# Kernel tuning notes

Measured on AMD Instinct MI355X. Metric: run time of the kernel, lower is better.

The kernel has to match this reference:

```python
import jax, jax.numpy as jnp
import numpy as np

N_USERS = 100000
N_ITEMS = 50000
N_NODES = N_USERS + N_ITEMS
NNZ = 1600000          # user-item interactions
EMBED_DIM = 64
N_LAYERS = 3
NORM_EPS = 1e-12       # F.normalize eps
DEG_EPS = 1e-07        # degree eps from module


def _build_graph():
    rng = np.random.default_rng(0)
    u = rng.integers(0, N_USERS, NNZ)
    v = rng.integers(0, N_ITEMS, NNZ)
    # dedupe (row, col) pairs so COO has unique entries, matching (A>0) degree logic
    pair = np.unique(u.astype(np.int64) * N_ITEMS + v.astype(np.int64))
    u = (pair // N_ITEMS).astype(np.int32)
    v = (pair % N_ITEMS).astype(np.int32)
    rows = np.concatenate([u, v + N_USERS]).astype(np.int32)
    cols = np.concatenate([v + N_USERS, u]).astype(np.int32)
    deg = np.bincount(rows, minlength=N_NODES).astype(np.float32)
    dinv = np.power(deg + DEG_EPS, -0.5).astype(np.float32)
    vals = dinv[rows] * dinv[cols]
    return rows, cols, vals


def setup_inputs() -> dict:
    key = jax.random.key(0)
    rows, cols, vals = _build_graph()
    in_embs = jax.random.normal(key, (N_NODES, EMBED_DIM), dtype=jnp.float32)
    return {
        "in_embs": in_embs,
        "rows": jnp.asarray(rows),
        "cols": jnp.asarray(cols),
        "vals": jnp.asarray(vals),
    }


def reference(in_embs, rows, cols, vals):
    n = in_embs.shape[0]
    x = in_embs
    out = in_embs
    for i in range(N_LAYERS):
        # SpMM: A_norm @ x  via edge gather + segment_sum scatter
        msg = vals[:, None] * x[cols]                      # [E, d]
        x = jax.ops.segment_sum(msg, rows, num_segments=n)  # [n, d]
        # F.normalize(x, dim=-1)
        norm = jnp.linalg.norm(x, axis=-1, keepdims=True)
        x = x / jnp.maximum(norm, NORM_EPS)
        out = out + x / (i + 1)
    return out
```

## Files before the change

### kernel.cpp

```cpp
#include <hip/hip_runtime.h>
#include <hip/hip_bf16.h>


constexpr int N_USERS = 100000;
constexpr int N_ITEMS = 50000;
constexpr int N_NODES = N_USERS + N_ITEMS;
constexpr int D = 64;
constexpr int NBK  = 196;
constexpr int SLOT = 12288;
constexpr int EPB  = 16384;

__device__ inline unsigned short f2bf(float f) {
    unsigned u = __float_as_uint(f);
    u += 0x7FFFu + ((u >> 16) & 1u);
    return (unsigned short)(u >> 16);
}
__device__ inline float bf2f(unsigned short h) {
    return __uint_as_float((unsigned)h << 16);
}

__global__ __launch_bounds__(256) void rpu_kernel(
    const int* __restrict__ rows, int* __restrict__ rpu, int Eh)
{
    int i = blockIdx.x * 256 + threadIdx.x;
    if (i > N_USERS) return;
    int lo = 0, hi = Eh;
    while (lo < hi) {
        int mid = (lo + hi) >> 1;
        if (rows[mid] < i) lo = mid + 1; else hi = mid;
    }
    rpu[i] = lo;
}

__global__ __launch_bounds__(256) void dinv_users(
    const int* __restrict__ rpu, float* __restrict__ dinv)
{
    int i = blockIdx.x * 256 + threadIdx.x;
    if (i < N_USERS)
        dinv[i] = rsqrtf((float)(rpu[i + 1] - rpu[i]) + 1e-7f);
}

__global__ __launch_bounds__(256) void init_cursors(int* __restrict__ bcur)
{
    int t = threadIdx.x;
    if (t < NBK) bcur[t] = t * SLOT;
}

__global__ __launch_bounds__(256) void bucket_scatter(
    const int* __restrict__ rows, const int* __restrict__ cols,
    int* __restrict__ bcur, int* __restrict__ staging, int Eh)
{
    __shared__ int hist[256];
    const int tid = threadIdx.x;
    const int base = blockIdx.x * EPB;
    const int nEdge = min(EPB, Eh - base);
    if (nEdge <= 0) return;

    hist[tid] = 0;
    __syncthreads();

    for (int s = 0; s < 16; ++s) {
        int o = s * 1024 + tid * 4;
        if (o + 3 < nEdge) {
            int4 c4 = *reinterpret_cast<const int4*>(cols + base + o);
            atomicAdd(&hist[(c4.x - N_USERS) >> 8], 1);
            atomicAdd(&hist[(c4.y - N_USERS) >> 8], 1);
            atomicAdd(&hist[(c4.z - N_USERS) >> 8], 1);
            atomicAdd(&hist[(c4.w - N_USERS) >> 8], 1);
        } else if (o < nEdge) {
            for (int k = o; k < nEdge; ++k)
                atomicAdd(&hist[(cols[base + k] - N_USERS) >> 8], 1);
        }
    }
    __syncthreads();

    if (tid < NBK) {
        int h = hist[tid];
        hist[tid] = (h > 0) ? atomicAdd(&bcur[tid], h) : 0;
    }
    __syncthreads();

    for (int s = 0; s < 16; ++s) {
        int o = s * 1024 + tid * 4;
        if (o + 3 < nEdge) {
            int4 c4 = *reinterpret_cast<const int4*>(cols + base + o);
            int4 u4 = *reinterpret_cast<const int4*>(rows + base + o);
            int v, p;
            v = c4.x - N_USERS; p = atomicAdd(&hist[v >> 8], 1);
            staging[p] = ((v & 255) << 24) | u4.x;
            v = c4.y - N_USERS; p = atomicAdd(&hist[v >> 8], 1);
            staging[p] = ((v & 255) << 24) | u4.y;
            v = c4.z - N_USERS; p = atomicAdd(&hist[v >> 8], 1);
            staging[p] = ((v & 255) << 24) | u4.z;
            v = c4.w - N_USERS; p = atomicAdd(&hist[v >> 8], 1);
            staging[p] = ((v & 255) << 24) | u4.w;
        } else if (o < nEdge) {
            for (int k = o; k < nEdge; ++k) {
                int v = cols[base + k] - N_USERS;
                int u = rows[base + k];
                int p = atomicAdd(&hist[v >> 8], 1);
                staging[p] = ((v & 255) << 24) | u;
            }
        }
    }
}

__global__ __launch_bounds__(256) void scan_buckets(
    const int* __restrict__ bcur, int* __restrict__ bbase, int* __restrict__ rpi)
{
    __shared__ int wsum[4];
    const int tid = threadIdx.x, lane = tid & 63, w = tid >> 6;
    int t = (tid < NBK) ? (bcur[tid] - tid * SLOT) : 0;
    int incl = t;
    #pragma unroll
    for (int off = 1; off < 64; off <<= 1) {
        int s = __shfl_up(incl, off);
        if (lane >= off) incl += s;
    }
    if (lane == 63) wsum[w] = incl;
    __syncthreads();
    int woff = 0;
    #pragma unroll
    for (int k = 0; k < 4; ++k) woff += (k < w) ? wsum[k] : 0;
    int excl = woff + incl - t;
    if (tid < NBK) bbase[tid] = excl;
    if (tid == NBK - 1) rpi[N_ITEMS] = excl + t;
}

__global__ __launch_bounds__(256) void item_csr(
    const int* __restrict__ bcur, const int* __restrict__ bbase,
    const int* __restrict__ staging, int* __restrict__ rpi,
    float* __restrict__ dinv, int* __restrict__ csr)
{
    __shared__ int hist[256];
    __shared__ int cur[256];
    __shared__ int wsum[4];
    const int b = blockIdx.x;
    const int tid = threadIdx.x, lane = tid & 63, w = tid >> 6;
    const int sbase = b * SLOT;
    const int n = bcur[b] - sbase;
    const int cbase = bbase[b];

    hist[tid] = 0;
    __syncthreads();
    for (int i = tid; i < n; i += 256)
        atomicAdd(&hist[((unsigned)staging[sbase + i]) >> 24], 1);
    __syncthreads();

    int h = hist[tid];
    int incl = h;
    #pragma unroll
    for (int off = 1; off < 64; off <<= 1) {
        int s = __shfl_up(incl, off);
        if (lane >= off) incl += s;
    }
    if (lane == 63) wsum[w] = incl;
    __syncthreads();
    int woff = 0;
    #pragma unroll
    for (int k = 0; k < 4; ++k) woff += (k < w) ? wsum[k] : 0;
    int excl = woff + incl - h;

    int gitem = b * 256 + tid;
    if (gitem < N_ITEMS) {
        rpi[gitem] = cbase + excl;
        dinv[N_USERS + gitem] = rsqrtf((float)h + 1e-7f);
    }
    cur[tid] = cbase + excl;
    __syncthreads();

    for (int i = tid; i < n; i += 256) {
        int e = staging[sbase + i];
        int p = atomicAdd(&cur[((unsigned)e) >> 24], 1);
        csr[p] = e & 0xFFFFFF;
    }
}

__global__ __launch_bounds__(256) void prep0(
    const float* __restrict__ init, const float* __restrict__ dinv,
    unsigned short* __restrict__ z)
{
    int i = blockIdx.x * 256 + threadIdx.x;
    if (i >= N_NODES * D / 4) return;
    int r = i >> 4;
    float dv = dinv[r];
    float4 x = reinterpret_cast<const float4*>(init)[i];
    ushort4 o;
    o.x = f2bf(x.x * dv); o.y = f2bf(x.y * dv);
    o.z = f2bf(x.z * dv); o.w = f2bf(x.w * dv);
    reinterpret_cast<ushort4*>(z)[i] = o;
}

__global__ __launch_bounds__(256) void spmm_norm(
    const unsigned short* __restrict__ z,
    const int* __restrict__ rpu,
    const int* __restrict__ rpi,
    const int* __restrict__ cols_u,
    const int* __restrict__ csr_col_i,
    const float* __restrict__ dinv,
    const float* __restrict__ init,
    unsigned short* __restrict__ zout,
    float* __restrict__ out,
    float invl, int first, int writez)
{
    const int tid = threadIdx.x;
    const int lane = tid & 63;
    const int g = lane >> 4;
    const int sl = lane & 15;
    const int wave = tid >> 6;
    const int row = blockIdx.x * 16 + wave * 4 + g;
    if (row >= N_NODES) return;
    const int gb = g << 4;

    int beg, end;
    const int* clist;
    if (row < N_USERS) {
        beg = rpu[row]; end = rpu[row + 1]; clist = cols_u;
    } else {
        int v = row - N_USERS;
        beg = rpi[v]; end = rpi[v + 1]; clist = csr_col_i;
    }

    float ax = 0.f, ay = 0.f, az = 0.f, aw = 0.f;
    for (int base = beg; base < end; base += 16) {
        int li = base + sl;
        int c_l = 0;
        if (li < end) c_l = clist[li];
        int nch = min(16, end - base);
        int j = 0;
        for (; j + 4 <= nch; j += 4) {
            int c0 = __shfl(c_l, gb + j + 0);
            int c1 = __shfl(c_l, gb + j + 1);
            int c2 = __shfl(c_l, gb + j + 2);
            int c3 = __shfl(c_l, gb + j + 3);
            ushort4 z0 = reinterpret_cast<const ushort4*>(z + (size_t)c0 * D)[sl];
            ushort4 z1 = reinterpret_cast<const ushort4*>(z + (size_t)c1 * D)[sl];
            ushort4 z2 = reinterpret_cast<const ushort4*>(z + (size_t)c2 * D)[sl];
            ushort4 z3 = reinterpret_cast<const ushort4*>(z + (size_t)c3 * D)[sl];
            ax += bf2f(z0.x); ay += bf2f(z0.y); az += bf2f(z0.z); aw += bf2f(z0.w);
            ax += bf2f(z1.x); ay += bf2f(z1.y); az += bf2f(z1.z); aw += bf2f(z1.w);
            ax += bf2f(z2.x); ay += bf2f(z2.y); az += bf2f(z2.z); aw += bf2f(z2.w);
            ax += bf2f(z3.x); ay += bf2f(z3.y); az += bf2f(z3.z); aw += bf2f(z3.w);
        }
        for (; j < nch; ++j) {
            int c = __shfl(c_l, gb + j);
            ushort4 zv = reinterpret_cast<const ushort4*>(z + (size_t)c * D)[sl];
            ax += bf2f(zv.x); ay += bf2f(zv.y); az += bf2f(zv.z); aw += bf2f(zv.w);
        }
    }

    float ss = ax * ax + ay * ay + az * az + aw * aw;
    #pragma unroll
    for (int off = 8; off > 0; off >>= 1)
        ss += __shfl_xor(ss, off);
    float nrm = sqrtf(ss);
    float rinv = 1.0f / fmaxf(nrm, 1e-12f);

    float xnx = ax * rinv, xny = ay * rinv, xnz = az * rinv, xnw = aw * rinv;

    size_t idx = (size_t)row * D + sl * 4;
    if (writez) {
        float dv = dinv[row];
        ushort4 zo;
        zo.x = f2bf(xnx * dv); zo.y = f2bf(xny * dv);
        zo.z = f2bf(xnz * dv); zo.w = f2bf(xnw * dv);
        reinterpret_cast<ushort4*>(zout + (size_t)row * D)[sl] = zo;
    }

    float4 bo = first ? *reinterpret_cast<const float4*>(init + idx)
                      : *reinterpret_cast<const float4*>(out + idx);
    bo.x += xnx * invl; bo.y += xny * invl;
    bo.z += xnz * invl; bo.w += xnw * invl;
    *reinterpret_cast<float4*>(out + idx) = bo;
}

extern "C" void kernel_launch(void* const* d_in, const int* in_sizes, int n_in,
                              void* d_out, int out_size, void* d_ws, size_t ws_size,
                              hipStream_t stream) {
    const float* in_embs = (const float*)d_in[0];
    const int*   rows    = (const int*)d_in[1];
    const int*   cols    = (const int*)d_in[2];
    float* out = (float*)d_out;

    const int E  = in_sizes[1];
    const int Eh = E / 2;
    const size_t z_bytes = (size_t)N_NODES * D * sizeof(unsigned short);

    auto align256 = [](size_t x) { return (x + 255) & ~(size_t)255; };
    char* p = (char*)d_ws;
    unsigned short* zP = (unsigned short*)p; p += align256(z_bytes);
    unsigned short* zQ = (unsigned short*)p; p += align256(z_bytes);
    int*   csr_col_i = (int*)p;   p += align256((size_t)Eh * sizeof(int));
    int*   rpu       = (int*)p;   p += align256((size_t)(N_USERS + 1) * sizeof(int));
    int*   rpi       = (int*)p;   p += align256((size_t)(N_ITEMS + 1) * sizeof(int));
    float* dinv      = (float*)p; p += align256((size_t)N_NODES * sizeof(float));
    int*   bcur      = (int*)p;   p += align256(256 * sizeof(int));
    int*   bbase     = (int*)p;   p += align256(256 * sizeof(int));
    int*   staging   = (int*)zP;

    init_cursors<<<1, 256, 0, stream>>>(bcur);
    bucket_scatter<<<(Eh + EPB - 1) / EPB, 256, 0, stream>>>(rows, cols, bcur, staging, Eh);
    scan_buckets<<<1, 256, 0, stream>>>(bcur, bbase, rpi);
    item_csr<<<NBK, 256, 0, stream>>>(bcur, bbase, staging, rpi, dinv, csr_col_i);
    rpu_kernel<<<(N_USERS + 256) / 256, 256, 0, stream>>>(rows, rpu, Eh);
    dinv_users<<<(N_USERS + 255) / 256, 256, 0, stream>>>(rpu, dinv);
    prep0<<<(N_NODES * D / 4 + 255) / 256, 256, 0, stream>>>(in_embs, dinv, zP);

    const int spmm_blocks = (N_NODES + 15) / 16;
    unsigned short* zin = zP;
    unsigned short* zout = zQ;
    for (int layer = 0; layer < 3; ++layer) {
        int last = (layer == 2);
        spmm_norm<<<spmm_blocks, 256, 0, stream>>>(
            zin, rpu, rpi, cols, csr_col_i, dinv, in_embs, zout, out,
            1.0f / (layer + 1), layer == 0 ? 1 : 0, last ? 0 : 1);
        unsigned short* t = zin; zin = zout; zout = t;
    }
}
```

Before: 250.7 us.

## Defer output accumulation to last layer, widen SpMM gathers, and fuse setup kernels

The SpMM kernel now assigns 8 lanes per row, each loading 16 bytes of bf16 features, so each gathered row takes fewer, wider memory instructions. The running fp32 output is no longer read and written after every layer. The final layer instead rebuilds the layer-1 and layer-2 embeddings from the stored bf16 z buffers by dividing out dinv, and writes the whole sum once. Several small setup kernels are merged: cursor init and user dinv move into rpu_kernel, and the bucket scan moves into item_csr. The cost is extra error, because the earlier layers' contributions now come from bf16 values scaled by 1/dinv rather than fp32.

```diff
diff --git a/kernel.cpp b/kernel.cpp
--- a/kernel.cpp
+++ b/kernel.cpp
@@ -10,40 +10,35 @@
 constexpr int SLOT = 12288;
 constexpr int EPB  = 16384;
 
-__device__ inline unsigned short f2bf(float f) {
+__device__ inline unsigned f2bf(float f) {
     unsigned u = __float_as_uint(f);
     u += 0x7FFFu + ((u >> 16) & 1u);
-    return (unsigned short)(u >> 16);
-}
-__device__ inline float bf2f(unsigned short h) {
-    return __uint_as_float((unsigned)h << 16);
+    return u >> 16;
+}
+__device__ inline float bflo(unsigned u) { return __uint_as_float(u << 16); }
+__device__ inline float bfhi(unsigned u) { return __uint_as_float(u & 0xFFFF0000u); }
+
+__device__ inline int lower_bound(const int* __restrict__ a, int n, int key) {
+    int lo = 0, hi = n;
+    while (lo < hi) { int m = (lo + hi) >> 1; if (a[m] < key) lo = m + 1; else hi = m; }
+    return lo;
 }
 
 __global__ __launch_bounds__(256) void rpu_kernel(
-    const int* __restrict__ rows, int* __restrict__ rpu, int Eh)
-{
+    const int* __restrict__ rows, int* __restrict__ rpu,
+    float* __restrict__ dinv, int* __restrict__ bcur, int Eh)
+{
+    if (blockIdx.x == 0 && threadIdx.x < NBK) bcur[threadIdx.x] = threadIdx.x * SLOT;
     int i = blockIdx.x * 256 + threadIdx.x;
     if (i > N_USERS) return;
-    int lo = 0, hi = Eh;
-    while (lo < hi) {
-        int mid = (lo + hi) >> 1;
-        if (rows[mid] < i) lo = mid + 1; else hi = mid;
-    }
+    int lo = lower_bound(rows, Eh, i);
     rpu[i] = lo;
-}
-
-__global__ __launch_bounds__(256) void dinv_users(
-    const int* __restrict__ rpu, float* __restrict__ dinv)
-{
-    int i = blockIdx.x * 256 + threadIdx.x;
+    int lane = threadIdx.x & 63;
+    int nxt = __shfl_down(lo, 1);
+    if (lane == 63 || i >= N_USERS)
+        nxt = (i < N_USERS) ? lower_bound(rows, Eh, i + 1) : lo;
     if (i < N_USERS)
-        dinv[i] = rsqrtf((float)(rpu[i + 1] - rpu[i]) + 1e-7f);
-}
-
-__global__ __launch_bounds__(256) void init_cursors(int* __restrict__ bcur)
-{
-    int t = threadIdx.x;
-    if (t < NBK) bcur[t] = t * SLOT;
+        dinv[i] = rsqrtf((float)(nxt - lo) + 1e-7f);
 }
 
 __global__ __launch_bounds__(256) void bucket_scatter(
@@ -105,13 +100,19 @@
     }
 }
 
-__global__ __launch_bounds__(256) void scan_buckets(
-    const int* __restrict__ bcur, int* __restrict__ bbase, int* __restrict__ rpi)
-{
+__global__ __launch_bounds__(256) void item_csr(
+    const int* __restrict__ bcur, const int* __restrict__ staging,
+    int* __restrict__ rpi, float* __restrict__ dinv, int* __restrict__ csr)
+{
+    __shared__ int hist[256];
+    __shared__ int cur[256];
     __shared__ int wsum[4];
+    __shared__ int s_cbase;
+    const int b = blockIdx.x;
     const int tid = threadIdx.x, lane = tid & 63, w = tid >> 6;
-    int t = (tid < NBK) ? (bcur[tid] - tid * SLOT) : 0;
-    int incl = t;
+
+    int tot = (tid < NBK) ? (bcur[tid] - tid * SLOT) : 0;
+    int incl = tot;
     #pragma unroll
     for (int off = 1; off < 64; off <<= 1) {
         int s = __shfl_up(incl, off);
@@ -122,24 +123,14 @@
     int woff = 0;
     #pragma unroll
     for (int k = 0; k < 4; ++k) woff += (k < w) ? wsum[k] : 0;
-    int excl = woff + incl - t;
-    if (tid < NBK) bbase[tid] = excl;
-    if (tid == NBK - 1) rpi[N_ITEMS] = excl + t;
-}
-
-__global__ __launch_bounds__(256) void item_csr(
-    const int* __restrict__ bcur, const int* __restrict__ bbase,
-    const int* __restrict__ staging, int* __restrict__ rpi,
-    float* __restrict__ dinv, int* __restrict__ csr)
-{
-    __shared__ int hist[256];
-    __shared__ int cur[256];
-    __shared__ int wsum[4];
-    const int b = blockIdx.x;
-    const int tid = threadIdx.x, lane = tid & 63, w = tid >> 6;
+    int excl = woff + incl - tot;
+    if (tid == b) s_cbase = excl;
+    if (b == 0 && tid == NBK - 1) rpi[N_ITEMS] = excl + tot;
+    __syncthreads();
+
     const int sbase = b * SLOT;
     const int n = bcur[b] - sbase;
-    const int cbase = bbase[b];
+    const int cbase = s_cbase;
 
     hist[tid] = 0;
     __syncthreads();
@@ -148,25 +139,25 @@
     __syncthreads();
 
     int h = hist[tid];
-    int incl = h;
+    int incl2 = h;
     #pragma unroll
     for (int off = 1; off < 64; off <<= 1) {
-        int s = __shfl_up(incl, off);
-        if (lane >= off) incl += s;
-    }
-    if (lane == 63) wsum[w] = incl;
-    __syncthreads();
-    int woff = 0;
+        int s = __shfl_up(incl2, off);
+        if (lane >= off) incl2 += s;
+    }
+    if (lane == 63) wsum[w] = incl2;
+    __syncthreads();
+    int woff2 = 0;
     #pragma unroll
-    for (int k = 0; k < 4; ++k) woff += (k < w) ? wsum[k] : 0;
-    int excl = woff + incl - h;
+    for (int k = 0; k < 4; ++k) woff2 += (k < w) ? wsum[k] : 0;
+    int excl2 = woff2 + incl2 - h;
 
     int gitem = b * 256 + tid;
     if (gitem < N_ITEMS) {
-        rpi[gitem] = cbase + excl;
+        rpi[gitem] = cbase + excl2;
         dinv[N_USERS + gitem] = rsqrtf((float)h + 1e-7f);
     }
-    cur[tid] = cbase + excl;
+    cur[tid] = cbase + excl2;
     __syncthreads();
 
     for (int i = tid; i < n; i += 256) {
@@ -185,32 +176,40 @@
     int r = i >> 4;
     float dv = dinv[r];
     float4 x = reinterpret_cast<const float4*>(init)[i];
-    ushort4 o;
-    o.x = f2bf(x.x * dv); o.y = f2bf(x.y * dv);
-    o.z = f2bf(x.z * dv); o.w = f2bf(x.w * dv);
-    reinterpret_cast<ushort4*>(z)[i] = o;
-}
-
-__global__ __launch_bounds__(256) void spmm_norm(
+    unsigned lo0 = f2bf(x.x * dv), hi0 = f2bf(x.y * dv);
+    unsigned lo1 = f2bf(x.z * dv), hi1 = f2bf(x.w * dv);
+    uint2 o; o.x = lo0 | (hi0 << 16); o.y = lo1 | (hi1 << 16);
+    reinterpret_cast<uint2*>(z)[i] = o;
+}
+
+#define ACC8(r) do { \
+    a0 += bflo(r.x); a1 += bfhi(r.x); \
+    a2 += bflo(r.y); a3 += bfhi(r.y); \
+    a4 += bflo(r.z); a5 += bfhi(r.z); \
+    a6 += bflo(r.w); a7 += bfhi(r.w); } while (0)
+
+template<int LAST>
+__global__ __launch_bounds__(256) void spmm8(
     const unsigned short* __restrict__ z,
     const int* __restrict__ rpu,
     const int* __restrict__ rpi,
     const int* __restrict__ cols_u,
     const int* __restrict__ csr_col_i,
     const float* __restrict__ dinv,
+    unsigned short* __restrict__ zout,
+    const unsigned short* z1,
+    const unsigned short* z2,
     const float* __restrict__ init,
-    unsigned short* __restrict__ zout,
-    float* __restrict__ out,
-    float invl, int first, int writez)
+    float* __restrict__ out)
 {
     const int tid = threadIdx.x;
     const int lane = tid & 63;
-    const int g = lane >> 4;
-    const int sl = lane & 15;
+    const int g  = lane >> 3;
+    const int sl = lane & 7;
     const int wave = tid >> 6;
-    const int row = blockIdx.x * 16 + wave * 4 + g;
+    const int row = blockIdx.x * 32 + wave * 8 + g;
     if (row >= N_NODES) return;
-    const int gb = g << 4;
+    const int gb = g << 3;
 
     int beg, end;
     const int* clist;
@@ -221,57 +220,74 @@
         beg = rpi[v]; end = rpi[v + 1]; clist = csr_col_i;
     }
 
-    float ax = 0.f, ay = 0.f, az = 0.f, aw = 0.f;
-    for (int base = beg; base < end; base += 16) {
-        int li = base + sl;
-        int c_l = 0;
-        if (li < end) c_l = clist[li];
-        int nch = min(16, end - base);
-        int j = 0;
-        for (; j + 4 <= nch; j += 4) {
-            int c0 = __shfl(c_l, gb + j + 0);
-            int c1 = __shfl(c_l, gb + j + 1);
-            int c2 = __shfl(c_l, gb + j + 2);
-            int c3 = __shfl(c_l, gb + j + 3);
-            ushort4 z0 = reinterpret_cast<const ushort4*>(z + (size_t)c0 * D)[sl];
-            ushort4 z1 = reinterpret_cast<const ushort4*>(z + (size_t)c1 * D)[sl];
-            ushort4 z2 = reinterpret_cast<const ushort4*>(z + (size_t)c2 * D)[sl];
-            ushort4 z3 = reinterpret_cast<const ushort4*>(z + (size_t)c3 * D)[sl];
-            ax += bf2f(z0.x); ay += bf2f(z0.y); az += bf2f(z0.z); aw += bf2f(z0.w);
-            ax += bf2f(z1.x); ay += bf2f(z1.y); az += bf2f(z1.z); aw += bf2f(z1.w);
-            ax += bf2f(z2.x); ay += bf2f(z2.y); az += bf2f(z2.z); aw += bf2f(z2.w);
-            ax += bf2f(z3.x); ay += bf2f(z3.y); az += bf2f(z3.z); aw += bf2f(z3.w);
+    float a0=0.f,a1=0.f,a2=0.f,a3=0.f,a4=0.f,a5=0.f,a6=0.f,a7=0.f;
+    const unsigned short* zs = z + (size_t)sl * 8;
+
+    int j = beg;
+    for (; j + 8 <= end; j += 8) {
+        int c_l = clist[j + sl];
+        int c0 = __shfl(c_l, gb + 0);
+        int c1 = __shfl(c_l, gb + 1);
+        int c2 = __shfl(c_l, gb + 2);
+        int c3 = __shfl(c_l, gb + 3);
+        int c4 = __shfl(c_l, gb + 4);
+        int c5 = __shfl(c_l, gb + 5);
+        int c6 = __shfl(c_l, gb + 6);
+        int c7 = __shfl(c_l, gb + 7);
+        uint4 r0 = *reinterpret_cast<const uint4*>(zs + (size_t)c0 * D);
+        uint4 r1 = *reinterpret_cast<const uint4*>(zs + (size_t)c1 * D);
+        uint4 r2 = *reinterpret_cast<const uint4*>(zs + (size_t)c2 * D);
+        uint4 r3 = *reinterpret_cast<const uint4*>(zs + (size_t)c3 * D);
+        uint4 r4 = *reinterpret_cast<const uint4*>(zs + (size_t)c4 * D);
+        uint4 r5 = *reinterpret_cast<const uint4*>(zs + (size_t)c5 * D);
+        uint4 r6 = *reinterpret_cast<const uint4*>(zs + (size_t)c6 * D);
+        uint4 r7 = *reinterpret_cast<const uint4*>(zs + (size_t)c7 * D);
+        ACC8(r0); ACC8(r1); ACC8(r2); ACC8(r3);
+        ACC8(r4); ACC8(r5); ACC8(r6); ACC8(r7);
+    }
+    int rem = end - j;
+    if (rem > 0) {
+        int c_l = (j + sl < end) ? clist[j + sl] : 0;
+        for (int k = 0; k < rem; ++k) {
+            int c = __shfl(c_l, gb + k);
+            uint4 r = *reinterpret_cast<const uint4*>(zs + (size_t)c * D);
+            ACC8(r);
         }
-        for (; j < nch; ++j) {
-            int c = __shfl(c_l, gb + j);
-            ushort4 zv = reinterpret_cast<const ushort4*>(z + (size_t)c * D)[sl];
-            ax += bf2f(zv.x); ay += bf2f(zv.y); az += bf2f(zv.z); aw += bf2f(zv.w);
-        }
-    }
-
-    float ss = ax * ax + ay * ay + az * az + aw * aw;
-    #pragma unroll
-    for (int off = 8; off > 0; off >>= 1)
-        ss += __shfl_xor(ss, off);
-    float nrm = sqrtf(ss);
-    float rinv = 1.0f / fmaxf(nrm, 1e-12f);
-
-    float xnx = ax * rinv, xny = ay * rinv, xnz = az * rinv, xnw = aw * rinv;
-
-    size_t idx = (size_t)row * D + sl * 4;
-    if (writez) {
-        float dv = dinv[row];
-        ushort4 zo;
-        zo.x = f2bf(xnx * dv); zo.y = f2bf(xny * dv);
-        zo.z = f2bf(xnz * dv); zo.w = f2bf(xnw * dv);
-        reinterpret_cast<ushort4*>(zout + (size_t)row * D)[sl] = zo;
-    }
-
-    float4 bo = first ? *reinterpret_cast<const float4*>(init + idx)
-                      : *reinterpret_cast<const float4*>(out + idx);
-    bo.x += xnx * invl; bo.y += xny * invl;
-    bo.z += xnz * invl; bo.w += xnw * invl;
-    *reinterpret_cast<float4*>(out + idx) = bo;
+    }
+
+    float ss = a0*a0 + a1*a1 + a2*a2 + a3*a3 + a4*a4 + a5*a5 + a6*a6 + a7*a7;
+    ss += __shfl_xor(ss, 1);
+    ss += __shfl_xor(ss, 2);
+    ss += __shfl_xor(ss, 4);
+    float rinv = 1.0f / fmaxf(sqrtf(ss), 1e-12f);
+
+    size_t idx = (size_t)row * D + (size_t)sl * 8;
+    if (!LAST) {
+        float s = rinv * dinv[row];
+        uint4 zo;
+        zo.x = f2bf(a0 * s) | (f2bf(a1 * s) << 16);
+        zo.y = f2bf(a2 * s) | (f2bf(a3 * s) << 16);
+        zo.z = f2bf(a4 * s) | (f2bf(a5 * s) << 16);
+        zo.w = f2bf(a6 * s) | (f2bf(a7 * s) << 16);
+        *reinterpret_cast<uint4*>(zout + idx) = zo;
+    } else {
+        float recip = 1.0f / dinv[row];
+        float k1 = recip, k2 = 0.5f * recip, k3 = rinv * (1.0f / 3.0f);
+        uint4 w1 = *reinterpret_cast<const uint4*>(z1 + idx);
+        uint4 w2 = *reinterpret_cast<const uint4*>(z2 + idx);
+        const float4* ip = reinterpret_cast<const float4*>(init + idx);
+        float4 o0 = ip[0], o1 = ip[1];
+        o0.x += bflo(w1.x) * k1 + bflo(w2.x) * k2 + a0 * k3;
+        o0.y += bfhi(w1.x) * k1 + bfhi(w2.x) * k2 + a1 * k3;
+        o0.z += bflo(w1.y) * k1 + bflo(w2.y) * k2 + a2 * k3;
+        o0.w += bfhi(w1.y) * k1 + bfhi(w2.y) * k2 + a3 * k3;
+        o1.x += bflo(w1.z) * k1 + bflo(w2.z) * k2 + a4 * k3;
+        o1.y += bfhi(w1.z) * k1 + bfhi(w2.z) * k2 + a5 * k3;
+        o1.z += bflo(w1.w) * k1 + bflo(w2.w) * k2 + a6 * k3;
+        o1.w += bfhi(w1.w) * k1 + bfhi(w2.w) * k2 + a7 * k3;
+        float4* op = reinterpret_cast<float4*>(out + idx);
+        op[0] = o0; op[1] = o1;
+    }
 }
 
 extern "C" void kernel_launch(void* const* d_in, const int* in_sizes, int n_in,
@@ -295,25 +311,18 @@
     int*   rpi       = (int*)p;   p += align256((size_t)(N_ITEMS + 1) * sizeof(int));
     float* dinv      = (float*)p; p += align256((size_t)N_NODES * sizeof(float));
     int*   bcur      = (int*)p;   p += align256(256 * sizeof(int));
-    int*   bbase     = (int*)p;   p += align256(256 * sizeof(int));
     int*   staging   = (int*)zP;
 
-    init_cursors<<<1, 256, 0, stream>>>(bcur);
+    rpu_kernel<<<(N_USERS + 256) / 256, 256, 0, stream>>>(rows, rpu, dinv, bcur, Eh);
     bucket_scatter<<<(Eh + EPB - 1) / EPB, 256, 0, stream>>>(rows, cols, bcur, staging, Eh);
-    scan_buckets<<<1, 256, 0, stream>>>(bcur, bbase, rpi);
-    item_csr<<<NBK, 256, 0, stream>>>(bcur, bbase, staging, rpi, dinv, csr_col_i);
-    rpu_kernel<<<(N_USERS + 256) / 256, 256, 0, stream>>>(rows, rpu, Eh);
-    dinv_users<<<(N_USERS + 255) / 256, 256, 0, stream>>>(rpu, dinv);
+    item_csr<<<NBK, 256, 0, stream>>>(bcur, staging, rpi, dinv, csr_col_i);
     prep0<<<(N_NODES * D / 4 + 255) / 256, 256, 0, stream>>>(in_embs, dinv, zP);
 
-    const int spmm_blocks = (N_NODES + 15) / 16;
-    unsigned short* zin = zP;
-    unsigned short* zout = zQ;
-    for (int layer = 0; layer < 3; ++layer) {
-        int last = (layer == 2);
-        spmm_norm<<<spmm_blocks, 256, 0, stream>>>(
-            zin, rpu, rpi, cols, csr_col_i, dinv, in_embs, zout, out,
-            1.0f / (layer + 1), layer == 0 ? 1 : 0, last ? 0 : 1);
-        unsigned short* t = zin; zin = zout; zout = t;
-    }
-}
+    const int grid = (N_NODES + 31) / 32;
+    spmm8<0><<<grid, 256, 0, stream>>>(zP, rpu, rpi, cols, csr_col_i, dinv,
+                                       zQ, nullptr, nullptr, nullptr, nullptr);
+    spmm8<0><<<grid, 256, 0, stream>>>(zQ, rpu, rpi, cols, csr_col_i, dinv,
+                                       zP, nullptr, nullptr, nullptr, nullptr);
+    spmm8<1><<<grid, 256, 0, stream>>>(zP, rpu, rpi, cols, csr_col_i, dinv,
+                                       nullptr, zQ, zP, in_embs, out);
+}
```

After: 226.8 us. -9.5%, faster.
